# Kernel optimization log

Hardware: AMD Instinct MI355X
Metric: run time of the kernel (lower is better)

## Reference

```python
import jax, jax.numpy as jnp
import numpy as np

DIM = 128        # per-head dim == model width in this module
Q_HEADS = 16
KV_HEADS = 4
WINDOW = 512
BATCH = 4
SEQ = 2048


def setup_inputs() -> dict:
    key = jax.random.key(0)
    k1, k2, k3 = jax.random.split(key, 3)
    x = jax.random.normal(k1, (BATCH, SEQ, DIM), dtype=jnp.float32)
    # fused qkv weight, stored (in, out) so forward is x @ W_qkv
    W_qkv = jax.random.normal(k2, (DIM, (Q_HEADS + 2 * KV_HEADS) * DIM), dtype=jnp.float32) * (DIM ** -0.5)
    W_proj = jax.random.normal(k3, (Q_HEADS * DIM, DIM), dtype=jnp.float32) * ((Q_HEADS * DIM) ** -0.5)
    return {"x": x, "W_qkv": W_qkv, "W_proj": W_proj}


def _gqa_forward(x, W_qkv, W_proj):
    b, s, d = x.shape
    qkv = x @ W_qkv                                    # [b, s, (Hq+2Hkv)*d]
    qkv = qkv.reshape(b, s, Q_HEADS + 2 * KV_HEADS, d).transpose(0, 2, 1, 3)
    q = qkv[:, :Q_HEADS]                               # [b, Hq, s, d]
    k = qkv[:, Q_HEADS:Q_HEADS + KV_HEADS]             # [b, Hkv, s, d]
    v = qkv[:, Q_HEADS + KV_HEADS:]                    # [b, Hkv, s, d]

    # GQA: repeat kv heads to match q heads
    group = Q_HEADS // KV_HEADS
    k = jnp.repeat(k, group, axis=1)                   # [b, Hq, s, d]
    v = jnp.repeat(v, group, axis=1)

    scale = 1.0 / jnp.sqrt(jnp.float32(d))
    scores = jnp.einsum('bhqd,bhkd->bhqk', q, k) * scale   # [b, Hq, s, s]

    q_idx = jnp.arange(s)[:, None]
    kv_idx = jnp.arange(s)[None, :]
    rel = (q_idx - kv_idx).astype(jnp.float32)         # [s, s]
    # per-head ALiBi slope: exp2(-(h+1)*8/Hq), added (sign matches source)
    h = jnp.arange(Q_HEADS, dtype=jnp.float32)
    slopes = jnp.exp2(-((h + 1.0) * 8.0 / Q_HEADS))    # [Hq]
    scores = scores + slopes[None, :, None, None] * rel[None, None, :, :]

    mask = (q_idx >= kv_idx) & ((q_idx - kv_idx) <= WINDOW)
    scores = jnp.where(mask[None, None], scores, -jnp.inf)
    probs = jax.nn.softmax(scores, axis=-1)

    att = jnp.einsum('bhqk,bhkd->bhqd', probs, v)      # [b, Hq, s, d]
    att = att.transpose(0, 2, 1, 3).reshape(b, s, Q_HEADS * d)
    return att @ W_proj                                # [b, s, d]


def reference(x, W_qkv, W_proj):
    return _gqa_forward(x, W_qkv, W_proj)
```

## Files before the change

### kernel.cpp

```cpp
#include <hip/hip_runtime.h>
#include <math.h>

#define DIM_    128
#define QH_     16
#define KVH_    4
#define WIN_    512
#define BATCH_  4
#define SEQ_    2048
#define QKV_LD  3072
#define ATT_LD  2048

#define NX   (BATCH_*SEQ_*DIM_)
#define NWQ  (DIM_*QKV_LD)
#define NWP  (ATT_LD*DIM_)

typedef __attribute__((ext_vector_type(8))) short short8;
typedef __attribute__((ext_vector_type(4))) float f32x4;
typedef unsigned short u16;
typedef unsigned int u32;

__device__ __forceinline__ u16 f2bf(float f) {
    u32 u = __float_as_uint(f);
    u += 0x7fff + ((u >> 16) & 1);
    return (u16)(u >> 16);
}
__device__ __forceinline__ float bf2f(u16 u) {
    return __uint_as_float(((u32)u) << 16);
}
__device__ __forceinline__ u32 pkbf(float a, float b) {
    u32 r;
    __asm__("v_cvt_pk_bf16_f32 %0, %1, %2" : "=v"(r) : "v"(a), "v"(b));
    return r;
}
#define MFMA16 __builtin_amdgcn_mfma_f32_16x16x32_bf16

#if __has_builtin(__builtin_amdgcn_exp2f)
#define EXP2F __builtin_amdgcn_exp2f
#else
#define EXP2F exp2f
#endif

__device__ __forceinline__ void gload_lds16(const u16* g, u16* l) {
    __builtin_amdgcn_global_load_lds(
        (const __attribute__((address_space(1))) unsigned int*)(const void*)g,
        (__attribute__((address_space(3))) unsigned int*)(void*)l, 16, 0, 0);
}

__global__ __launch_bounds__(256) void prep(
    const float* __restrict__ x, const float* __restrict__ Wqkv,
    const float* __restrict__ Wproj,
    u16* __restrict__ xh, u16* __restrict__ wth, u16* __restrict__ wpth)
{
    if (blockIdx.x < 1024) {
        const size_t t = (size_t)blockIdx.x * 256 + threadIdx.x;
        float4 v = *(const float4*)(x + 4 * t);
        ushort4 o;
        o.x = f2bf(v.x); o.y = f2bf(v.y); o.z = f2bf(v.z); o.w = f2bf(v.w);
        *(ushort4*)(xh + 4 * t) = o;
        return;
    }
    __shared__ float T[32][33];
    int tile = blockIdx.x - 1024;
    const float* src; u16* dst; int K, N;
    if (tile < 384) { src = Wqkv;  dst = wth;  K = 128;  N = 3072; }
    else { tile -= 384; src = Wproj; dst = wpth; K = 2048; N = 128; }
    const int ntile = N >> 5;
    const int k0 = (tile / ntile) << 5, n0 = (tile % ntile) << 5;
    const int tx = threadIdx.x & 31, ty = threadIdx.x >> 5;
    #pragma unroll
    for (int i = 0; i < 4; ++i)
        T[ty + 8 * i][tx] = src[(size_t)(k0 + ty + 8 * i) * N + n0 + tx];
    __syncthreads();
    #pragma unroll
    for (int i = 0; i < 4; ++i)
        dst[(size_t)(n0 + ty + 8 * i) * K + k0 + tx] = f2bf(T[tx][ty + 8 * i]);
}

__global__ __launch_bounds__(256) void gemm1_mfma(
    const u16* __restrict__ xh, const u16* __restrict__ wth,
    u16* __restrict__ qkvb, u16* __restrict__ vg)
{
    __shared__ u16 Ab[32][512];
    __shared__ u16 Bb[16][512];
    const int bn = blockIdx.x * 64;
    const int bm = blockIdx.y * 128;
    const int tid = threadIdx.x;
    const int wv = tid >> 6, lane = tid & 63;
    const int lr = lane & 15, quad = lane >> 4;
    const int lo = lane & 15, hi = lane >> 4;

    #pragma unroll
    for (int i = 0; i < 12; ++i) {
        const int idx = wv * 12 + i;
        if (idx < 32) {
            const int mt = idx >> 2, s = idx & 3;
            gload_lds16(xh + (size_t)(bm + mt * 16 + lo) * DIM_ + s * 32 + hi * 8,
                        &Ab[idx][0]);
        } else {
            const int j = idx - 32, nt = j >> 2, s = j & 3;
            gload_lds16(wth + (size_t)(bn + nt * 16 + lo) * DIM_ + s * 32 + hi * 8,
                        &Bb[j][0]);
        }
    }
    __syncthreads();

    const int wr = wv >> 1, wc = wv & 1;
    f32x4 acc[4][2] = {};
    if (bn < 2560) {
        #pragma unroll
        for (int s = 0; s < 4; ++s) {
            short8 af[4], bf[2];
            #pragma unroll
            for (int mt = 0; mt < 4; ++mt)
                af[mt] = *(const short8*)&Ab[(wr * 4 + mt) * 4 + s][lane * 8];
            #pragma unroll
            for (int nt = 0; nt < 2; ++nt)
                bf[nt] = *(const short8*)&Bb[(wc * 2 + nt) * 4 + s][lane * 8];
            #pragma unroll
            for (int mt = 0; mt < 4; ++mt)
                #pragma unroll
                for (int nt = 0; nt < 2; ++nt)
                    acc[mt][nt] = MFMA16(bf[nt], af[mt], acc[mt][nt], 0, 0, 0);
        }
        #pragma unroll
        for (int mt = 0; mt < 4; ++mt)
            #pragma unroll
            for (int nt = 0; nt < 2; ++nt) {
                uint2 o;
                o.x = pkbf(acc[mt][nt][0], acc[mt][nt][1]);
                o.y = pkbf(acc[mt][nt][2], acc[mt][nt][3]);
                *(uint2*)(qkvb
                    + (size_t)(bm + wr * 64 + mt * 16 + lr) * QKV_LD
                    + bn + wc * 32 + nt * 16 + quad * 4) = o;
            }
    } else {
        #pragma unroll
        for (int s = 0; s < 4; ++s) {
            short8 af[4], bf[2];
            #pragma unroll
            for (int mt = 0; mt < 4; ++mt)
                af[mt] = *(const short8*)&Ab[(wr * 4 + mt) * 4 + s][lane * 8];
            #pragma unroll
            for (int nt = 0; nt < 2; ++nt)
                bf[nt] = *(const short8*)&Bb[(wc * 2 + nt) * 4 + s][lane * 8];
            #pragma unroll
            for (int mt = 0; mt < 4; ++mt)
                #pragma unroll
                for (int nt = 0; nt < 2; ++nt)
                    acc[mt][nt] = MFMA16(af[mt], bf[nt], acc[mt][nt], 0, 0, 0);
        }
        #pragma unroll
        for (int mt = 0; mt < 4; ++mt)
            #pragma unroll
            for (int nt = 0; nt < 2; ++nt) {
                const int ncol = bn + wc * 32 + nt * 16 + lr - 2560;
                const int kvh = ncol >> 7, d = ncol & 127;
                const int m0 = bm + wr * 64 + mt * 16 + quad * 4;
                uint2 o;
                o.x = pkbf(acc[mt][nt][0], acc[mt][nt][1]);
                o.y = pkbf(acc[mt][nt][2], acc[mt][nt][3]);
                *(uint2*)(vg + ((size_t)((m0 >> 11) * KVH_ + kvh) * DIM_ + d)
                            * SEQ_ + (m0 & 2047)) = o;
            }
    }
}

__global__ __launch_bounds__(256, 4) void attn_mfma(
    const u16* __restrict__ qkvb, const u16* __restrict__ vg,
    u16* __restrict__ ah)
{
    const int xcd  = blockIdx.x & 7;
    const int idx  = blockIdx.x >> 3;
    const int pair = xcd + 8 * (idx & 1);
    const int qt   = idx >> 1;
    const int b    = pair >> 2, kvh = pair & 3;
    const int q0 = qt << 4;
    const int tid = threadIdx.x;
    const int wv = tid >> 6, lane = tid & 63;
    const int lr = lane & 15, quad = lane >> 4;
    const int h = kvh * 4 + wv;

    __shared__ u16 Kb[2][8][512];
    __shared__ u16 Vb[2][8][512];
    __shared__ u16 Pt[4][16][36];

    const float scale2 = 0.08838834764831845f * 1.4426950408889634f;
    const float slope2 = exp2f(-0.5f * (float)(h + 1)) * 1.4426950408889634f;
    const int jbase = max(0, q0 - WIN_);
    const int nch = (q0 + 16 - jbase + 31) >> 5;
    const size_t rowb = (size_t)b * SEQ_;
    const u16* kg  = qkvb + rowb * QKV_LD + (QH_ + kvh) * DIM_;
    const u16* vgb = vg + (size_t)(b * KVH_ + kvh) * DIM_ * SEQ_;
    const int lo = lane & 15, hi = lane >> 4;

    short8 qf[4];
    {
        const u16* qp = qkvb + (rowb + q0 + lr) * QKV_LD + h * DIM_ + quad * 8;
        #pragma unroll
        for (int s = 0; s < 4; ++s) qf[s] = *(const short8*)(qp + 32 * s);
    }

    float alpha0;
    {
        const int q = q0 + lr;
        const int rm = (q < WIN_) ? q : WIN_;
        alpha0 = slope2 * (float)(q - rm);
    }

    f32x4 O[8] = {};
    float rs = 0.f;

    #define STAGE(CH, SLOT) do {                                              \
        const int _jk0 = jbase + ((CH) << 5);                                 \
        const int _jk = (_jk0 < SEQ_ - 32) ? _jk0 : (SEQ_ - 32);              \
        _Pragma("unroll")                                                     \
        for (int _t = 0; _t < 2; ++_t) {                                      \
            const int _p = wv + _t * 4;                                       \
            gload_lds16(kg + (size_t)(_jk + (_p >> 2) * 16 + lo) * QKV_LD     \
                        + (_p & 3) * 32 + hi * 8, &Kb[(SLOT)][_p][0]);        \
            gload_lds16(vgb + (size_t)(_p * 16 + lo) * SEQ_ + _jk + hi * 8,   \
                        &Vb[(SLOT)][_p][0]);                                  \
        }                                                                     \
    } while (0)

    STAGE(0, 0);

    for (int ch = 0; ch < nch; ++ch) {
        const int jk = jbase + (ch << 5);
        const int slot = ch & 1;
        { const int cn = (ch + 1 < nch) ? (ch + 1) : (nch - 1);
          STAGE(cn, slot ^ 1); }
        __asm__ volatile("s_waitcnt vmcnt(4)" ::: "memory");
        __asm__ volatile("s_barrier" ::: "memory");

        #pragma unroll
        for (int nt = 0; nt < 2; ++nt) {
            f32x4 c0 = {0.f, 0.f, 0.f, 0.f};
            #pragma unroll
            for (int s = 0; s < 4; ++s) {
                short8 kf = *(const short8*)&Kb[slot][nt * 4 + s][lane * 8];
                c0 = MFMA16(kf, qf[s], c0, 0, 0, 0);
            }
            const int jknt = jk + nt * 16;
            const float b0 = fmaf(-slope2, (float)(jknt + quad * 4), alpha0);
            float e0, e1, e2, e3;
            if (q0 >= jknt + 15 && q0 + 15 <= jknt + WIN_) {
                e0 = EXP2F(fmaf(c0[0], scale2, b0));
                e1 = EXP2F(fmaf(c0[1], scale2, b0 - slope2));
                e2 = EXP2F(fmaf(c0[2], scale2, b0 - 2.f * slope2));
                e3 = EXP2F(fmaf(c0[3], scale2, b0 - 3.f * slope2));
            } else {
                const int q = q0 + lr, j0q = jknt + quad * 4;
                float ee[4];
                #pragma unroll
                for (int r = 0; r < 4; ++r) {
                    const int rel = q - (j0q + r);
                    const float t = fmaf(c0[r], scale2, b0 - (float)r * slope2);
                    ee[r] = ((unsigned)rel <= (unsigned)WIN_) ? EXP2F(t) : 0.f;
                }
                e0 = ee[0]; e1 = ee[1]; e2 = ee[2]; e3 = ee[3];
            }
            rs += (e0 + e1) + (e2 + e3);
            uint2 o;
            o.x = pkbf(e0, e1);
            o.y = pkbf(e2, e3);
            *(uint2*)&Pt[wv][lr][nt * 16 + quad * 4] = o;
        }
        __asm__ volatile("s_waitcnt lgkmcnt(0)" ::: "memory");

        short8 pa0 = *(const short8*)&Pt[wv][lr][quad * 8];
        #pragma unroll
        for (int nt = 0; nt < 8; ++nt) {
            short8 vf = *(const short8*)&Vb[slot][nt][lane * 8];
            O[nt] = MFMA16(vf, pa0, O[nt], 0, 0, 0);
        }
        __asm__ volatile("s_barrier" ::: "memory");
    }
    #undef STAGE

    __asm__ volatile("s_waitcnt vmcnt(0)" ::: "memory");

    rs += __shfl_xor(rs, 16);
    rs += __shfl_xor(rs, 32);

    {
        const float inv = 1.0f / rs;
        u16* dst = ah + (rowb + q0 + lr) * (size_t)ATT_LD + h * DIM_;
        #pragma unroll
        for (int nt = 0; nt < 8; ++nt) {
            uint2 o;
            o.x = pkbf(O[nt][0] * inv, O[nt][1] * inv);
            o.y = pkbf(O[nt][2] * inv, O[nt][3] * inv);
            *(uint2*)(dst + nt * 16 + quad * 4) = o;
        }
    }
}

__global__ __launch_bounds__(256) void gemm2_mfma(
    const u16* __restrict__ ah, const u16* __restrict__ wpth,
    float* __restrict__ out)
{
    const int bm = blockIdx.x * 16;
    const int wv = threadIdx.x >> 6, lane = threadIdx.x & 63;
    const int lr = lane & 15, quad = lane >> 4;
    const int cq = wv;

    const u16* arow  = ah + (size_t)(bm + lr) * ATT_LD + quad * 8;
    const u16* w0row = wpth + (size_t)(cq * 32 + lr) * ATT_LD + quad * 8;
    const u16* w1row = w0row + (size_t)16 * ATT_LD;

    f32x4 acc0 = {0.f, 0.f, 0.f, 0.f}, acc1 = {0.f, 0.f, 0.f, 0.f};
    #pragma unroll 8
    for (int k0 = 0; k0 < ATT_LD; k0 += 32) {
        short8 a  = *(const short8*)(arow + k0);
        short8 w0 = *(const short8*)(w0row + k0);
        short8 w1 = *(const short8*)(w1row + k0);
        acc0 = MFMA16(w0, a, acc0, 0, 0, 0);
        acc1 = MFMA16(w1, a, acc1, 0, 0, 0);
    }
    float* orow = out + (size_t)(bm + lr) * DIM_ + cq * 32;
    *(float4*)(orow + quad * 4)      = *(float4*)&acc0;
    *(float4*)(orow + 16 + quad * 4) = *(float4*)&acc1;
}

extern "C" void kernel_launch(void* const* d_in, const int* in_sizes, int n_in,
                              void* d_out, int out_size, void* d_ws, size_t ws_size,
                              hipStream_t stream)
{
    const float* x     = (const float*)d_in[0];
    const float* Wqkv  = (const float*)d_in[1];
    const float* Wproj = (const float*)d_in[2];
    float* out = (float*)d_out;

    u16* xh   = (u16*)d_ws;
    u16* wth  = xh   + (size_t)NX;
    u16* wpth = wth  + (size_t)NWQ;
    u16* qkvb = wpth + (size_t)NWP;
    u16* vg   = qkvb + (size_t)8192 * QKV_LD;
    u16* ahp  = vg   + (size_t)BATCH_ * KVH_ * DIM_ * SEQ_;

    prep<<<1024 + 640, 256, 0, stream>>>(x, Wqkv, Wproj, xh, wth, wpth);

    gemm1_mfma<<<dim3(QKV_LD / 64, 8192 / 128), 256, 0, stream>>>(
        xh, wth, qkvb, vg);

    attn_mfma<<<2048, 256, 0, stream>>>(qkvb, vg, ahp);

    gemm2_mfma<<<8192 / 16, 256, 0, stream>>>(ahp, wpth, out);
}
```

Baseline: 212.2 us.

## Enlarge attention query tile to 64 rows with triple-buffered K/V staging

Each attention block now processes 64 query rows per wave (four 16-row MFMA tiles) instead of 16. Every K/V chunk loaded into LDS is therefore reused across four times as many queries, which cuts global and LDS traffic per query and the redundant loading of window overlap. The K/V buffers go from double to triple buffering with a prefetch distance of two, and the trailing barrier is removed. In exchange register pressure rises (occupancy hint drops to 2), the grid shrinks to 512 blocks, and there is more masked work at the diagonal and window edges.

```diff
diff --git a/kernel.cpp b/kernel.cpp
--- a/kernel.cpp
+++ b/kernel.cpp
@@ -165,7 +165,7 @@
     }
 }
 
-__global__ __launch_bounds__(256, 4) void attn_mfma(
+__global__ __launch_bounds__(256, 2) void attn_mfma(
     const u16* __restrict__ qkvb, const u16* __restrict__ vg,
     u16* __restrict__ ah)
 {
@@ -174,45 +174,47 @@
     const int pair = xcd + 8 * (idx & 1);
     const int qt   = idx >> 1;
     const int b    = pair >> 2, kvh = pair & 3;
-    const int q0 = qt << 4;
+    const int q0 = qt << 6;
     const int tid = threadIdx.x;
     const int wv = tid >> 6, lane = tid & 63;
     const int lr = lane & 15, quad = lane >> 4;
     const int h = kvh * 4 + wv;
 
-    __shared__ u16 Kb[2][8][512];
-    __shared__ u16 Vb[2][8][512];
-    __shared__ u16 Pt[4][16][36];
+    __shared__ u16 Kb[3][8][512];
+    __shared__ u16 Vb[3][8][512];
+    __shared__ u16 Pt[4][64][36];
 
     const float scale2 = 0.08838834764831845f * 1.4426950408889634f;
     const float slope2 = exp2f(-0.5f * (float)(h + 1)) * 1.4426950408889634f;
     const int jbase = max(0, q0 - WIN_);
-    const int nch = (q0 + 16 - jbase + 31) >> 5;
+    const int nch = (q0 + 64 - jbase) >> 5;
     const size_t rowb = (size_t)b * SEQ_;
     const u16* kg  = qkvb + rowb * QKV_LD + (QH_ + kvh) * DIM_;
     const u16* vgb = vg + (size_t)(b * KVH_ + kvh) * DIM_ * SEQ_;
     const int lo = lane & 15, hi = lane >> 4;
 
-    short8 qf[4];
-    {
-        const u16* qp = qkvb + (rowb + q0 + lr) * QKV_LD + h * DIM_ + quad * 8;
-        #pragma unroll
-        for (int s = 0; s < 4; ++s) qf[s] = *(const short8*)(qp + 32 * s);
-    }
-
-    float alpha0;
-    {
-        const int q = q0 + lr;
+    short8 qf[4][4];
+    #pragma unroll
+    for (int m = 0; m < 4; ++m) {
+        const u16* qp = qkvb + (rowb + q0 + m * 16 + lr) * QKV_LD
+                        + h * DIM_ + quad * 8;
+        #pragma unroll
+        for (int s = 0; s < 4; ++s) qf[m][s] = *(const short8*)(qp + 32 * s);
+    }
+
+    float alpha[4];
+    #pragma unroll
+    for (int m = 0; m < 4; ++m) {
+        const int q = q0 + m * 16 + lr;
         const int rm = (q < WIN_) ? q : WIN_;
-        alpha0 = slope2 * (float)(q - rm);
-    }
-
-    f32x4 O[8] = {};
-    float rs = 0.f;
+        alpha[m] = slope2 * (float)(q - rm);
+    }
+
+    f32x4 O[4][8] = {};
+    float rs[4] = {0.f, 0.f, 0.f, 0.f};
 
     #define STAGE(CH, SLOT) do {                                              \
-        const int _jk0 = jbase + ((CH) << 5);                                 \
-        const int _jk = (_jk0 < SEQ_ - 32) ? _jk0 : (SEQ_ - 32);              \
+        const int _jk = jbase + ((CH) << 5);                                  \
         _Pragma("unroll")                                                     \
         for (int _t = 0; _t < 2; ++_t) {                                      \
             const int _p = wv + _t * 4;                                       \
@@ -224,73 +226,89 @@
     } while (0)
 
     STAGE(0, 0);
+    STAGE(1, 1);
 
     for (int ch = 0; ch < nch; ++ch) {
         const int jk = jbase + (ch << 5);
-        const int slot = ch & 1;
-        { const int cn = (ch + 1 < nch) ? (ch + 1) : (nch - 1);
-          STAGE(cn, slot ^ 1); }
+        const int slot = ch % 3;
         __asm__ volatile("s_waitcnt vmcnt(4)" ::: "memory");
         __asm__ volatile("s_barrier" ::: "memory");
+        { const int cn = (ch + 2 < nch) ? (ch + 2) : (nch - 1);
+          STAGE(cn, (ch + 2) % 3); }
 
         #pragma unroll
         for (int nt = 0; nt < 2; ++nt) {
-            f32x4 c0 = {0.f, 0.f, 0.f, 0.f};
+            f32x4 c[4] = {};
             #pragma unroll
             for (int s = 0; s < 4; ++s) {
                 short8 kf = *(const short8*)&Kb[slot][nt * 4 + s][lane * 8];
-                c0 = MFMA16(kf, qf[s], c0, 0, 0, 0);
+                #pragma unroll
+                for (int m = 0; m < 4; ++m)
+                    c[m] = MFMA16(kf, qf[m][s], c[m], 0, 0, 0);
             }
             const int jknt = jk + nt * 16;
-            const float b0 = fmaf(-slope2, (float)(jknt + quad * 4), alpha0);
-            float e0, e1, e2, e3;
-            if (q0 >= jknt + 15 && q0 + 15 <= jknt + WIN_) {
-                e0 = EXP2F(fmaf(c0[0], scale2, b0));
-                e1 = EXP2F(fmaf(c0[1], scale2, b0 - slope2));
-                e2 = EXP2F(fmaf(c0[2], scale2, b0 - 2.f * slope2));
-                e3 = EXP2F(fmaf(c0[3], scale2, b0 - 3.f * slope2));
-            } else {
-                const int q = q0 + lr, j0q = jknt + quad * 4;
-                float ee[4];
-                #pragma unroll
-                for (int r = 0; r < 4; ++r) {
-                    const int rel = q - (j0q + r);
-                    const float t = fmaf(c0[r], scale2, b0 - (float)r * slope2);
-                    ee[r] = ((unsigned)rel <= (unsigned)WIN_) ? EXP2F(t) : 0.f;
+            const float bq = -slope2 * (float)(jknt + quad * 4);
+            #pragma unroll
+            for (int m = 0; m < 4; ++m) {
+                const int qm0 = q0 + m * 16;
+                const float b0 = bq + alpha[m];
+                float e0, e1, e2, e3;
+                if (qm0 >= jknt + 15 && qm0 + 15 <= jknt + WIN_) {
+                    e0 = EXP2F(fmaf(c[m][0], scale2, b0));
+                    e1 = EXP2F(fmaf(c[m][1], scale2, b0 - slope2));
+                    e2 = EXP2F(fmaf(c[m][2], scale2, b0 - 2.f * slope2));
+                    e3 = EXP2F(fmaf(c[m][3], scale2, b0 - 3.f * slope2));
+                } else {
+                    const int q = qm0 + lr, j0q = jknt + quad * 4;
+                    float ee[4];
+                    #pragma unroll
+                    for (int r = 0; r < 4; ++r) {
+                        const int rel = q - (j0q + r);
+                        const float t = fmaf(c[m][r], scale2, b0 - (float)r * slope2);
+                        ee[r] = ((unsigned)rel <= (unsigned)WIN_) ? EXP2F(t) : 0.f;
+                    }
+                    e0 = ee[0]; e1 = ee[1]; e2 = ee[2]; e3 = ee[3];
                 }
-                e0 = ee[0]; e1 = ee[1]; e2 = ee[2]; e3 = ee[3];
+                rs[m] += (e0 + e1) + (e2 + e3);
+                uint2 o;
+                o.x = pkbf(e0, e1);
+                o.y = pkbf(e2, e3);
+                *(uint2*)&Pt[wv][m * 16 + lr][nt * 16 + quad * 4] = o;
             }
-            rs += (e0 + e1) + (e2 + e3);
-            uint2 o;
-            o.x = pkbf(e0, e1);
-            o.y = pkbf(e2, e3);
-            *(uint2*)&Pt[wv][lr][nt * 16 + quad * 4] = o;
         }
         __asm__ volatile("s_waitcnt lgkmcnt(0)" ::: "memory");
 
-        short8 pa0 = *(const short8*)&Pt[wv][lr][quad * 8];
+        short8 pa[4];
+        #pragma unroll
+        for (int m = 0; m < 4; ++m)
+            pa[m] = *(const short8*)&Pt[wv][m * 16 + lr][quad * 8];
         #pragma unroll
         for (int nt = 0; nt < 8; ++nt) {
             short8 vf = *(const short8*)&Vb[slot][nt][lane * 8];
-            O[nt] = MFMA16(vf, pa0, O[nt], 0, 0, 0);
-        }
-        __asm__ volatile("s_barrier" ::: "memory");
+            #pragma unroll
+            for (int m = 0; m < 4; ++m)
+                O[m][nt] = MFMA16(vf, pa[m], O[m][nt], 0, 0, 0);
+        }
     }
     #undef STAGE
 
     __asm__ volatile("s_waitcnt vmcnt(0)" ::: "memory");
 
-    rs += __shfl_xor(rs, 16);
-    rs += __shfl_xor(rs, 32);
-
-    {
-        const float inv = 1.0f / rs;
-        u16* dst = ah + (rowb + q0 + lr) * (size_t)ATT_LD + h * DIM_;
+    #pragma unroll
+    for (int m = 0; m < 4; ++m) {
+        rs[m] += __shfl_xor(rs[m], 16);
+        rs[m] += __shfl_xor(rs[m], 32);
+    }
+
+    #pragma unroll
+    for (int m = 0; m < 4; ++m) {
+        const float inv = 1.0f / rs[m];
+        u16* dst = ah + (rowb + q0 + m * 16 + lr) * (size_t)ATT_LD + h * DIM_;
         #pragma unroll
         for (int nt = 0; nt < 8; ++nt) {
             uint2 o;
-            o.x = pkbf(O[nt][0] * inv, O[nt][1] * inv);
-            o.y = pkbf(O[nt][2] * inv, O[nt][3] * inv);
+            o.x = pkbf(O[m][nt][0] * inv, O[m][nt][1] * inv);
+            o.y = pkbf(O[m][nt][2] * inv, O[m][nt][3] * inv);
             *(uint2*)(dst + nt * 16 + quad * 4) = o;
         }
     }
@@ -344,7 +362,7 @@
     gemm1_mfma<<<dim3(QKV_LD / 64, 8192 / 128), 256, 0, stream>>>(
         xh, wth, qkvb, vg);
 
-    attn_mfma<<<2048, 256, 0, stream>>>(qkvb, vg, ahp);
+    attn_mfma<<<512, 256, 0, stream>>>(qkvb, vg, ahp);
 
     gemm2_mfma<<<8192 / 16, 256, 0, stream>>>(ahp, wpth, out);
 }
```

After: 228.5 us. +7.7%, slower.

## Widen attention blocks to 32 queries, triple-buffer KV, swap P via permlane

Applied to the files above, without the earlier changes.

The attention kernel now uses 512-thread blocks that each cover 32 query rows (two 16-row halves per head), so every K/V chunk staged in LDS serves twice as many queries and the grid is halved. KV staging moves to a three-slot ring with a two-chunk prefetch, which removes the trailing barrier. The probability tile is rebuilt in registers with permlane32_swap and shuffles instead of going through an LDS round trip. MFMA sections are wrapped in s_setprio to favour matrix issue. This adds LDS footprint and register pressure, and lowers the number of resident blocks.

```diff
diff --git a/kernel.cpp b/kernel.cpp
--- a/kernel.cpp
+++ b/kernel.cpp
@@ -165,7 +165,7 @@
     }
 }
 
-__global__ __launch_bounds__(256, 4) void attn_mfma(
+__global__ __launch_bounds__(512) void attn_mfma(
     const u16* __restrict__ qkvb, const u16* __restrict__ vg,
     u16* __restrict__ ah)
 {
@@ -174,20 +174,21 @@
     const int pair = xcd + 8 * (idx & 1);
     const int qt   = idx >> 1;
     const int b    = pair >> 2, kvh = pair & 3;
-    const int q0 = qt << 4;
+    const int q0 = qt << 5;
     const int tid = threadIdx.x;
-    const int wv = tid >> 6, lane = tid & 63;
+    const int wv8 = tid >> 6, lane = tid & 63;
+    const int hq = wv8 >> 1, mrow = wv8 & 1;
     const int lr = lane & 15, quad = lane >> 4;
-    const int h = kvh * 4 + wv;
-
-    __shared__ u16 Kb[2][8][512];
-    __shared__ u16 Vb[2][8][512];
-    __shared__ u16 Pt[4][16][36];
+    const int h = kvh * 4 + hq;
+    const bool oddq = (quad & 1) != 0;
+
+    __shared__ u16 Kb[3][8][512];
+    __shared__ u16 Vb[3][8][512];
 
     const float scale2 = 0.08838834764831845f * 1.4426950408889634f;
     const float slope2 = exp2f(-0.5f * (float)(h + 1)) * 1.4426950408889634f;
     const int jbase = max(0, q0 - WIN_);
-    const int nch = (q0 + 16 - jbase + 31) >> 5;
+    const int nch = (q0 + 32 - jbase) >> 5;
     const size_t rowb = (size_t)b * SEQ_;
     const u16* kg  = qkvb + rowb * QKV_LD + (QH_ + kvh) * DIM_;
     const u16* vgb = vg + (size_t)(b * KVH_ + kvh) * DIM_ * SEQ_;
@@ -195,14 +196,15 @@
 
     short8 qf[4];
     {
-        const u16* qp = qkvb + (rowb + q0 + lr) * QKV_LD + h * DIM_ + quad * 8;
+        const u16* qp = qkvb + (rowb + q0 + mrow * 16 + lr) * QKV_LD
+                        + h * DIM_ + quad * 8;
         #pragma unroll
         for (int s = 0; s < 4; ++s) qf[s] = *(const short8*)(qp + 32 * s);
     }
 
     float alpha0;
     {
-        const int q = q0 + lr;
+        const int q = q0 + mrow * 16 + lr;
         const int rm = (q < WIN_) ? q : WIN_;
         alpha0 = slope2 * (float)(q - rm);
     }
@@ -211,70 +213,83 @@
     float rs = 0.f;
 
     #define STAGE(CH, SLOT) do {                                              \
-        const int _jk0 = jbase + ((CH) << 5);                                 \
-        const int _jk = (_jk0 < SEQ_ - 32) ? _jk0 : (SEQ_ - 32);              \
-        _Pragma("unroll")                                                     \
-        for (int _t = 0; _t < 2; ++_t) {                                      \
-            const int _p = wv + _t * 4;                                       \
-            gload_lds16(kg + (size_t)(_jk + (_p >> 2) * 16 + lo) * QKV_LD     \
-                        + (_p & 3) * 32 + hi * 8, &Kb[(SLOT)][_p][0]);        \
-            gload_lds16(vgb + (size_t)(_p * 16 + lo) * SEQ_ + _jk + hi * 8,   \
-                        &Vb[(SLOT)][_p][0]);                                  \
-        }                                                                     \
+        const int _jk = jbase + ((CH) << 5);                                  \
+        gload_lds16(kg + (size_t)(_jk + (wv8 >> 2) * 16 + lo) * QKV_LD        \
+                    + (wv8 & 3) * 32 + hi * 8, &Kb[(SLOT)][wv8][0]);          \
+        gload_lds16(vgb + (size_t)(wv8 * 16 + lo) * SEQ_ + _jk + hi * 8,      \
+                    &Vb[(SLOT)][wv8][0]);                                     \
     } while (0)
 
     STAGE(0, 0);
+    STAGE(1, 1);
 
     for (int ch = 0; ch < nch; ++ch) {
         const int jk = jbase + (ch << 5);
-        const int slot = ch & 1;
-        { const int cn = (ch + 1 < nch) ? (ch + 1) : (nch - 1);
-          STAGE(cn, slot ^ 1); }
-        __asm__ volatile("s_waitcnt vmcnt(4)" ::: "memory");
+        const int slot = ch % 3;
+        __asm__ volatile("s_waitcnt vmcnt(2)" ::: "memory");
         __asm__ volatile("s_barrier" ::: "memory");
-
+        { const int cn = (ch + 2 < nch) ? (ch + 2) : (nch - 1);
+          STAGE(cn, (ch + 2) % 3); }
+
+        u32 pw[2][2];
+        const int qm0 = q0 + mrow * 16;
         #pragma unroll
         for (int nt = 0; nt < 2; ++nt) {
-            f32x4 c0 = {0.f, 0.f, 0.f, 0.f};
+            f32x4 c = {0.f, 0.f, 0.f, 0.f};
+            __builtin_amdgcn_s_setprio(1);
             #pragma unroll
             for (int s = 0; s < 4; ++s) {
                 short8 kf = *(const short8*)&Kb[slot][nt * 4 + s][lane * 8];
-                c0 = MFMA16(kf, qf[s], c0, 0, 0, 0);
-            }
+                c = MFMA16(kf, qf[s], c, 0, 0, 0);
+            }
+            __builtin_amdgcn_s_setprio(0);
             const int jknt = jk + nt * 16;
             const float b0 = fmaf(-slope2, (float)(jknt + quad * 4), alpha0);
             float e0, e1, e2, e3;
-            if (q0 >= jknt + 15 && q0 + 15 <= jknt + WIN_) {
-                e0 = EXP2F(fmaf(c0[0], scale2, b0));
-                e1 = EXP2F(fmaf(c0[1], scale2, b0 - slope2));
-                e2 = EXP2F(fmaf(c0[2], scale2, b0 - 2.f * slope2));
-                e3 = EXP2F(fmaf(c0[3], scale2, b0 - 3.f * slope2));
+            if (qm0 >= jknt + 15 && qm0 + 15 <= jknt + WIN_) {
+                e0 = EXP2F(fmaf(c[0], scale2, b0));
+                e1 = EXP2F(fmaf(c[1], scale2, b0 - slope2));
+                e2 = EXP2F(fmaf(c[2], scale2, b0 - 2.f * slope2));
+                e3 = EXP2F(fmaf(c[3], scale2, b0 - 3.f * slope2));
             } else {
-                const int q = q0 + lr, j0q = jknt + quad * 4;
+                const int q = qm0 + lr, j0q = jknt + quad * 4;
                 float ee[4];
                 #pragma unroll
                 for (int r = 0; r < 4; ++r) {
                     const int rel = q - (j0q + r);
-                    const float t = fmaf(c0[r], scale2, b0 - (float)r * slope2);
+                    const float t = fmaf(c[r], scale2, b0 - (float)r * slope2);
                     ee[r] = ((unsigned)rel <= (unsigned)WIN_) ? EXP2F(t) : 0.f;
                 }
                 e0 = ee[0]; e1 = ee[1]; e2 = ee[2]; e3 = ee[3];
             }
             rs += (e0 + e1) + (e2 + e3);
-            uint2 o;
-            o.x = pkbf(e0, e1);
-            o.y = pkbf(e2, e3);
-            *(uint2*)&Pt[wv][lr][nt * 16 + quad * 4] = o;
-        }
-        __asm__ volatile("s_waitcnt lgkmcnt(0)" ::: "memory");
-
-        short8 pa0 = *(const short8*)&Pt[wv][lr][quad * 8];
+            pw[nt][0] = pkbf(e0, e1);
+            pw[nt][1] = pkbf(e2, e3);
+        }
+
+        short8 pa;
+        {
+            union { u32 w[4]; short8 s; } P;
+            #pragma unroll
+            for (int w = 0; w < 2; ++w) {
+                auto r = __builtin_amdgcn_permlane32_swap(
+                    pw[0][w], pw[1][w], false, false);
+                const u32 rx = r[0], ry = r[1];
+                const u32 sx = (u32)__shfl_xor((int)rx, 16);
+                const u32 sy = (u32)__shfl_xor((int)ry, 16);
+                P.w[w]     = oddq ? sy : rx;
+                P.w[2 + w] = oddq ? ry : sx;
+            }
+            pa = P.s;
+        }
+
+        __builtin_amdgcn_s_setprio(1);
         #pragma unroll
         for (int nt = 0; nt < 8; ++nt) {
             short8 vf = *(const short8*)&Vb[slot][nt][lane * 8];
-            O[nt] = MFMA16(vf, pa0, O[nt], 0, 0, 0);
-        }
-        __asm__ volatile("s_barrier" ::: "memory");
+            O[nt] = MFMA16(vf, pa, O[nt], 0, 0, 0);
+        }
+        __builtin_amdgcn_s_setprio(0);
     }
     #undef STAGE
 
@@ -285,7 +300,8 @@
 
     {
         const float inv = 1.0f / rs;
-        u16* dst = ah + (rowb + q0 + lr) * (size_t)ATT_LD + h * DIM_;
+        u16* dst = ah + (rowb + q0 + mrow * 16 + lr) * (size_t)ATT_LD
+                   + h * DIM_;
         #pragma unroll
         for (int nt = 0; nt < 8; ++nt) {
             uint2 o;
@@ -344,7 +360,7 @@
     gemm1_mfma<<<dim3(QKV_LD / 64, 8192 / 128), 256, 0, stream>>>(
         xh, wth, qkvb, vg);
 
-    attn_mfma<<<2048, 256, 0, stream>>>(qkvb, vg, ahp);
+    attn_mfma<<<1024, 512, 0, stream>>>(qkvb, vg, ahp);
 
     gemm2_mfma<<<8192 / 16, 256, 0, stream>>>(ahp, wpth, out);
 }
```

Result: faster. 201.5 us (-5.0%).
